# Kernel tuning notes

Measured on AMD Instinct MI355X. Metric: run time of the kernel, lower is better.

## Reference

```python
import jax, jax.numpy as jnp
import numpy as np

B, T, W, HP = 1, 64, 88, 48   # batch, frames, pitches, hidden_per_pitch
NU, NH, K = 24, 4, 25          # n_unit, n_heads, neighborhood window
HD = NU // NH                  # head dim = 6
HL = NU // 2                   # LSTM hidden per direction = 12


def _lstm_bidir(x, w_ih, w_hh, b_ih, b_hh):
    # x: [N, T, In]; w_ih: [2, 4*HL, In]; w_hh: [2, 4*HL, HL]; biases: [2, 4*HL]
    N = x.shape[0]
    def run(Wih, Whh, bih, bhh, reverse):
        def step(carry, xt):
            h, c = carry
            g = xt @ Wih.T + h @ Whh.T + bih + bhh
            i, f, gg, o = jnp.split(g, 4, axis=-1)  # torch gate order i,f,g,o
            c = jax.nn.sigmoid(f) * c + jax.nn.sigmoid(i) * jnp.tanh(gg)
            h = jax.nn.sigmoid(o) * jnp.tanh(c)
            return (h, c), h
        init = (jnp.zeros((N, HL), x.dtype), jnp.zeros((N, HL), x.dtype))
        _, ys = jax.lax.scan(step, init, jnp.swapaxes(x, 0, 1), reverse=reverse)
        return jnp.swapaxes(ys, 0, 1)
    return jnp.concatenate([run(w_ih[0], w_hh[0], b_ih[0], b_hh[0], False),
                            run(w_ih[1], w_hh[1], b_ih[1], b_hh[1], True)], axis=-1)


def _natten2d(x, qkv_w, qkv_b, rpb, proj_w, proj_b):
    # Neighborhood attention over 2D grid [B, Hh, Ww] with KxK window clamped at borders.
    Bn, Hh, Ww, C = x.shape
    qkv = (x @ qkv_w.T + qkv_b).reshape(Bn, Hh, Ww, 3, NH, HD)
    q = qkv[..., 0, :, :] * (HD ** -0.5)
    k = qkv[..., 1, :, :]
    v = qkv[..., 2, :, :]
    half = K // 2
    ar = jnp.arange(K)
    idx_i = jnp.clip(jnp.arange(Hh) - half, 0, Hh - K)[:, None] + ar  # [Hh,K]
    idx_j = jnp.clip(jnp.arange(Ww) - half, 0, Ww - K)[:, None] + ar  # [Ww,K]
    kg = k[:, idx_i][:, :, :, idx_j]  # [B,Hh,K,Ww,K,NH,HD]
    vg = v[:, idx_i][:, :, :, idx_j]
    ri = idx_i - jnp.arange(Hh)[:, None] + (K - 1)  # relative pos bias indices [Hh,K]
    rj = idx_j - jnp.arange(Ww)[:, None] + (K - 1)  # [Ww,K]
    bias = rpb[:, ri][:, :, :, rj]                  # [NH,Hh,K,Ww,K]
    logits = jnp.einsum('bijnd,biajcnd->bnijac', q, kg)
    logits = logits + jnp.transpose(bias, (0, 1, 3, 2, 4))[None]
    attn = jax.nn.softmax(logits.reshape(Bn, NH, Hh, Ww, K * K), axis=-1)
    attn = attn.reshape(Bn, NH, Hh, Ww, K, K)
    out = jnp.einsum('bnijac,biajcnd->bijnd', attn, vg).reshape(Bn, Hh, Ww, C)
    return out @ proj_w.T + proj_b


def _forward(features, condition, mask, emb, w_ih_l0, w_hh_l0, b_ih_l0, b_hh_l0,
             w_ih_l1, w_hh_l1, b_ih_l1, b_hh_l1, qkv_w, qkv_b, rpb, proj_w, proj_b,
             out_w, out_b):
    # concat: [B,T,88,HP] + [B,T,88,4] + [B,T,88,1] -> [B,T,88,HP+5]
    cat = jnp.concatenate([jnp.transpose(features, (0, 1, 3, 2)), emb[condition],
                           mask[..., None]], axis=-1)
    x = jnp.transpose(cat, (0, 2, 1, 3)).reshape(B * W, T, HP + 5)  # pitchwise LSTM
    x = _lstm_bidir(x, w_ih_l0, w_hh_l0, b_ih_l0, b_hh_l0)
    x = _lstm_bidir(x, w_ih_l1, w_hh_l1, b_ih_l1, b_hh_l1)
    x = jnp.transpose(x.reshape(B, W, T, NU), (0, 2, 1, 3))  # [B,T,88,NU]
    for _ in range(2):  # n_layers=2; Sequential(*[m]*2) => SHARED weights
        x = _natten2d(x, qkv_w, qkv_b, rpb, proj_w, proj_b)
    return x @ out_w.T + out_b  # [B,T,88,5]


def setup_inputs():
    ks = jax.random.split(jax.random.key(0), 24)
    def unif(k, shape, fan):
        s = 1.0 / np.sqrt(fan)
        return jax.random.uniform(k, shape, jnp.float32, -s, s)
    return {
        'features': jax.random.normal(ks[0], (B, T, HP, W), jnp.float32),
        'condition': jax.random.randint(ks[1], (B, T, W), 0, 5),
        'mask': jax.random.uniform(ks[2], (B, T, W), jnp.float32),
        'emb': jax.random.normal(ks[3], (5, 4), jnp.float32),
        'w_ih_l0': unif(ks[4], (2, 4 * HL, HP + 5), HL),
        'w_hh_l0': unif(ks[5], (2, 4 * HL, HL), HL),
        'b_ih_l0': unif(ks[6], (2, 4 * HL), HL),
        'b_hh_l0': unif(ks[7], (2, 4 * HL), HL),
        'w_ih_l1': unif(ks[8], (2, 4 * HL, 2 * HL), HL),
        'w_hh_l1': unif(ks[9], (2, 4 * HL, HL), HL),
        'b_ih_l1': unif(ks[10], (2, 4 * HL), HL),
        'b_hh_l1': unif(ks[11], (2, 4 * HL), HL),
        'qkv_w': unif(ks[12], (3 * NU, NU), NU),
        'qkv_b': unif(ks[13], (3 * NU,), NU),
        'rpb': jax.random.normal(ks[14], (NH, 2 * K - 1, 2 * K - 1), jnp.float32) * 0.02,
        'proj_w': unif(ks[15], (NU, NU), NU),
        'proj_b': unif(ks[16], (NU,), NU),
        'out_w': unif(ks[17], (5, NU), NU),
        'out_b': unif(ks[18], (5,), NU),
    }


def reference(features, condition, mask, emb, w_ih_l0, w_hh_l0, b_ih_l0, b_hh_l0,
              w_ih_l1, w_hh_l1, b_ih_l1, b_hh_l1, qkv_w, qkv_b, rpb, proj_w, proj_b,
              out_w, out_b):
    return _forward(features, condition, mask, emb, w_ih_l0, w_hh_l0, b_ih_l0, b_hh_l0,
                    w_ih_l1, w_hh_l1, b_ih_l1, b_hh_l1, qkv_w, qkv_b, rpb,
                    proj_w, proj_b, out_w, out_b)
```

## Files before the change

### kernel.cpp

```cpp
#include <hip/hip_runtime.h>
#include <hip/hip_bf16.h>

#define NPIX (64*88)
#define NSEQ 88
#define TT 64
#define F0 53
#define GATES 48

typedef __hip_bfloat16 bf16;

__device__ __forceinline__ float frcp(float x){ return __builtin_amdgcn_rcpf(x); }

__device__ __forceinline__ void unpack6(uint4 r, float* f){
  f[0] = __uint_as_float(r.x << 16);
  f[1] = __uint_as_float(r.x & 0xffff0000u);
  f[2] = __uint_as_float(r.y << 16);
  f[3] = __uint_as_float(r.y & 0xffff0000u);
  f[4] = __uint_as_float(r.z << 16);
  f[5] = __uint_as_float(r.z & 0xffff0000u);
}

__global__ __launch_bounds__(1024) void k_core(
    const float* __restrict__ feat, const int* __restrict__ cond,
    const float* __restrict__ mask, const float* __restrict__ emb,
    const float* __restrict__ wih0, const float* __restrict__ whh0,
    const float* __restrict__ bih0, const float* __restrict__ bhh0,
    const float* __restrict__ wih1, const float* __restrict__ whh1,
    const float* __restrict__ bih1, const float* __restrict__ bhh1,
    const float* __restrict__ qkv_w, const float* __restrict__ qkv_b,
    float* __restrict__ q, bf16* __restrict__ kh, bf16* __restrict__ vh){
  int n = blockIdx.x; int tid = threadIdx.x;
  int wave = tid >> 6; int lane = tid & 63;
  __shared__ float smem[14816];
  float* gbuf = smem;
  float* sx   = smem + 6144;
  float* sw0  = smem + 6144+3392;
  float* w1   = smem + 6144;
  float* sqkv = smem + 6144+2400;
  float* y0   = smem + 6144+4200;
  float* y1   = smem + 6144+5736;
  float* bsum = smem + 14624;

  for (int idx = tid; idx < 2*GATES*F0; idx += 1024) sw0[idx] = wih0[idx];
  for (int idx = tid; idx < TT*F0; idx += 1024){
    int t = idx / F0, f = idx - t*F0;
    float v;
    if (f < 48)      v = feat[(t*48 + f)*88 + n];
    else if (f < 52) v = emb[cond[t*88+n]*4 + (f-48)];
    else             v = mask[t*88+n];
    sx[idx] = v;
  }
  if (tid < 96)       bsum[tid] = bih0[tid] + bhh0[tid];
  else if (tid < 192) bsum[tid] = bih1[tid-96] + bhh1[tid-96];
  __syncthreads();

  #pragma unroll
  for (int r = 0; r < 6; ++r){
    int row = tid + r*1024;
    int d = row / 3072; int rem = row - d*3072;
    int t = rem / 48; int j = rem - t*48;
    const float* xr = sx + t*F0;
    const float* wr = sw0 + (d*GATES + j)*F0;
    float a0=0.f, a1=0.f, a2=0.f, a3=0.f;
    #pragma unroll
    for (int f=0; f<52; f+=4){
      a0 += xr[f  ]*wr[f  ];
      a1 += xr[f+1]*wr[f+1];
      a2 += xr[f+2]*wr[f+2];
      a3 += xr[f+3]*wr[f+3];
    }
    gbuf[(d*TT + t)*GATES + j] = bsum[d*GATES+j] + xr[52]*wr[52] + ((a0+a1)+(a2+a3));
  }
  __syncthreads();

  if (wave >= 2){
    for (int idx = tid-128; idx < 2*GATES*24; idx += 896){
      int row = idx / 24, f = idx - row*24;
      w1[row*25 + f] = wih1[idx];
    }
    for (int idx = tid-128; idx < 72*24; idx += 896){
      int row = idx / 24, f = idx - row*24;
      sqkv[row*25 + f] = qkv_w[idx];
    }
  } else {
    int d = wave;
    int j = (lane < GATES) ? lane : (lane - GATES);
    int u = j % 12; int grp = j / 12;
    float w[12];
    const float* wb = whh0 + (d*GATES + j)*12;
    #pragma unroll
    for (int m=0;m<12;++m) w[m] = wb[m];
    float negs  = (grp==2) ? -2.f : -1.f;
    float amul  = (grp==2) ?  2.f :  1.f;
    float aadd  = (grp==2) ? -1.f :  0.f;
    const float* gb = gbuf + d*TT*GATES + j;
    float hval = 0.f, cval = 0.f;
    int t0 = d ? (TT-1) : 0;
    float gnext = gb[t0*GATES];
    for (int s=0;s<TT;++s){
      int t = d ? (TT-1-s) : s;
      float gg = gnext;
      int tn = d ? max(TT-2-s,0) : min(s+1,TT-1);
      gnext = gb[tn*GATES];
      float h0=__shfl(hval,0), h1=__shfl(hval,1), h2=__shfl(hval,2);
      float h3=__shfl(hval,3), h4=__shfl(hval,4), h5=__shfl(hval,5);
      float h6=__shfl(hval,6), h7=__shfl(hval,7), h8=__shfl(hval,8);
      float h9=__shfl(hval,9), h10=__shfl(hval,10), h11=__shfl(hval,11);
      float a0 = gg + h0*w[0] + h4*w[4] + h8*w[8];
      float a1 = h1*w[1] + h5*w[5] + h9*w[9];
      float a2 = h2*w[2] + h6*w[6] + h10*w[10];
      float a3 = h3*w[3] + h7*w[7] + h11*w[11];
      float dot = (a0+a1)+(a2+a3);
      float act = amul*frcp(1.f + __expf(negs*dot)) + aadd;
      float ai = __shfl(act, u);
      float af = __shfl(act, u+12);
      float ag = __shfl(act, u+24);
      float ao = __shfl(act, u+36);
      float cn = af*cval + ai*ag;
      float th = 2.f*frcp(1.f + __expf(-2.f*cn)) - 1.f;
      hval = ao*th; cval = cn;
      if (lane < 12) y0[t*24 + d*12 + lane] = hval;
    }
  }
  __syncthreads();

  #pragma unroll
  for (int r = 0; r < 6; ++r){
    int row = tid + r*1024;
    int d = row / 3072; int rem = row - d*3072;
    int t = rem / 48; int j = rem - t*48;
    const float* xr = y0 + t*24;
    const float* wr = w1 + (d*GATES + j)*25;
    float a0=0.f, a1=0.f;
    #pragma unroll
    for (int c=0; c<24; c+=2){ a0 += xr[c]*wr[c]; a1 += xr[c+1]*wr[c+1]; }
    gbuf[(d*TT + t)*GATES + j] = bsum[96 + d*GATES+j] + a0 + a1;
  }
  __syncthreads();

  if (wave < 2){
    int d = wave;
    int j = (lane < GATES) ? lane : (lane - GATES);
    int u = j % 12; int grp = j / 12;
    float w[12];
    const float* wb = whh1 + (d*GATES + j)*12;
    #pragma unroll
    for (int m=0;m<12;++m) w[m] = wb[m];
    float negs  = (grp==2) ? -2.f : -1.f;
    float amul  = (grp==2) ?  2.f :  1.f;
    float aadd  = (grp==2) ? -1.f :  0.f;
    const float* gb = gbuf + d*TT*GATES + j;
    float hval = 0.f, cval = 0.f;
    int t0 = d ? (TT-1) : 0;
    float gnext = gb[t0*GATES];
    for (int s=0;s<TT;++s){
      int t = d ? (TT-1-s) : s;
      float gg = gnext;
      int tn = d ? max(TT-2-s,0) : min(s+1,TT-1);
      gnext = gb[tn*GATES];
      float h0=__shfl(hval,0), h1=__shfl(hval,1), h2=__shfl(hval,2);
      float h3=__shfl(hval,3), h4=__shfl(hval,4), h5=__shfl(hval,5);
      float h6=__shfl(hval,6), h7=__shfl(hval,7), h8=__shfl(hval,8);
      float h9=__shfl(hval,9), h10=__shfl(hval,10), h11=__shfl(hval,11);
      float a0 = gg + h0*w[0] + h4*w[4] + h8*w[8];
      float a1 = h1*w[1] + h5*w[5] + h9*w[9];
      float a2 = h2*w[2] + h6*w[6] + h10*w[10];
      float a3 = h3*w[3] + h7*w[7] + h11*w[11];
      float dot = (a0+a1)+(a2+a3);
      float act = amul*frcp(1.f + __expf(negs*dot)) + aadd;
      float ai = __shfl(act, u);
      float af = __shfl(act, u+12);
      float ag = __shfl(act, u+24);
      float ao = __shfl(act, u+36);
      float cn = af*cval + ai*ag;
      float th = 2.f*frcp(1.f + __expf(-2.f*cn)) - 1.f;
      hval = ao*th; cval = cn;
      if (lane < 12) y1[t*24 + d*12 + lane] = hval;
    }
  }
  __syncthreads();

  for (int idx = tid; idx < TT*72; idx += 1024){
    int gq = idx % 72; int t = idx / 72;
    int p = t*88 + n;
    const float* xr = y1 + t*24;
    const float* wr = sqkv + gq*25;
    float a0=0.f, a1=0.f;
    #pragma unroll
    for (int c=0; c<24; c+=2){ a0 += xr[c]*wr[c]; a1 += xr[c+1]*wr[c+1]; }
    float acc = qkv_b[gq] + a0 + a1;
    int s = gq/24, rem = gq - s*24;
    if (s==0) q[p*24+rem] = acc*0.4082482904638631f;
    else {
      int hh = rem/6, pos = rem - hh*6;
      bf16* dst = (s==1) ? kh : vh;
      dst[((size_t)hh*NPIX + p)*8 + pos] = __float2bfloat16(acc);
    }
  }
}

__global__ __launch_bounds__(512) void k_attn(
    const float* __restrict__ q, const bf16* __restrict__ kh,
    const bf16* __restrict__ vh, const float* __restrict__ rpb,
    float* __restrict__ ao){
  int b = blockIdx.x;
  int h = b / 704; int rem = b - h*704;
  int ti = rem / 44, tj = rem - ti*44;
  int i0 = ti*4, j0 = tj*2;
  int tid = threadIdx.x;
  int w = tid >> 6; int lane = tid & 63;
  int osi = min(max(i0-12,0),39);
  int osj = min(max(j0-12,0),63);

  __shared__ uint4 kt[28*26];
  __shared__ uint4 vt[28*26];
  const uint4* kg = (const uint4*)(kh + (size_t)h*NPIX*8);
  const uint4* vg = (const uint4*)(vh + (size_t)h*NPIX*8);
  for (int idx = tid; idx < 28*26; idx += 512){
    int a = idx / 26, cc = idx - a*26;
    int gi = min(osi + a, 63), gj = min(osj + cc, 87);
    int src = gi*88 + gj;
    kt[idx] = kg[src];
    vt[idx] = vg[src];
  }
  __syncthreads();

  int pi = i0 + (w>>1), pj = j0 + (w&1);
  int p = pi*88 + pj;
  int dsi = min(max(pi-12,0),39) - osi;
  int dsj = min(max(pj-12,0),63) - osj;
  int rbi = osi + dsi - pi + 24;
  int rbj = osj + dsj - pj + 24;

  float qv[6];
  #pragma unroll
  for (int d=0; d<6; ++d) qv[d] = q[p*24 + h*6 + d];

  float lgv[10]; int rof[10];
  float lmax = -1e30f;
  #pragma unroll
  for (int it=0; it<10; ++it){
    int nb = lane + it*64;
    bool valid = nb < 625;
    int nbc = valid ? nb : 624;
    int a = nbc/25, cc = nbc - a*25;
    int r = (a+dsi)*26 + (cc+dsj);
    rof[it] = r;
    float kr[6];
    unpack6(kt[r], kr);
    float lg = qv[0]*kr[0]+qv[1]*kr[1]+qv[2]*kr[2]+qv[3]*kr[3]+qv[4]*kr[4]+qv[5]*kr[5];
    lg += rpb[(h*49 + (a + rbi))*49 + (cc + rbj)];
    lg = valid ? lg : -1e30f;
    lgv[it] = lg;
    lmax = fmaxf(lmax, lg);
  }
  #pragma unroll
  for (int off=32; off; off>>=1) lmax = fmaxf(lmax, __shfl_xor(lmax, off));
  float lsum = 0.f;
  #pragma unroll
  for (int it=0; it<10; ++it){
    float pe = __expf(lgv[it]-lmax);
    lgv[it] = pe; lsum += pe;
  }
  #pragma unroll
  for (int off=32; off; off>>=1) lsum += __shfl_xor(lsum, off);
  float acc[6] = {0,0,0,0,0,0};
  #pragma unroll
  for (int it=0; it<10; ++it){
    float vr[6];
    unpack6(vt[rof[it]], vr);
    float pe = lgv[it];
    #pragma unroll
    for (int d=0; d<6; ++d) acc[d] += pe*vr[d];
  }
  #pragma unroll
  for (int d=0; d<6; ++d){
    #pragma unroll
    for (int off=32; off; off>>=1) acc[d] += __shfl_xor(acc[d], off);
  }
  if (lane == 0){
    float inv = frcp(lsum);
    #pragma unroll
    for (int d=0; d<6; ++d) ao[p*24 + h*6 + d] = acc[d]*inv;
  }
}

__global__ __launch_bounds__(64) void k_proj_qkv(const float* __restrict__ ain,
    const float* __restrict__ pw, const float* __restrict__ pb,
    const float* __restrict__ qkv_w, const float* __restrict__ qkv_b,
    float* __restrict__ q2, bf16* __restrict__ kh2, bf16* __restrict__ vh2){
  int p = blockIdx.x; int tid = threadIdx.x;
  __shared__ float arow[24];
  __shared__ float xrow[24];
  if (tid < 24) arow[tid] = ain[p*24+tid];
  __syncthreads();
  if (tid < 24){
    float a2 = pb[tid];
    const float* wr = pw + tid*24;
    #pragma unroll
    for (int c=0;c<24;++c) a2 += arow[c]*wr[c];
    xrow[tid] = a2;
  }
  __syncthreads();
  for (int g = tid; g < 72; g += 64){
    float a2 = qkv_b[g];
    const float* wr = qkv_w + g*24;
    #pragma unroll
    for (int c=0;c<24;++c) a2 += xrow[c]*wr[c];
    int s = g/24, rem = g - s*24;
    if (s==0) q2[p*24+rem] = a2*0.4082482904638631f;
    else {
      int hh = rem/6, pos = rem - hh*6;
      bf16* dst = (s==1) ? kh2 : vh2;
      dst[((size_t)hh*NPIX + p)*8 + pos] = __float2bfloat16(a2);
    }
  }
}

__global__ __launch_bounds__(64) void k_proj_out(const float* __restrict__ ain,
    const float* __restrict__ pw, const float* __restrict__ pb,
    const float* __restrict__ ow, const float* __restrict__ ob,
    float* __restrict__ out){
  int p = blockIdx.x; int tid = threadIdx.x;
  __shared__ float arow[24];
  __shared__ float xrow[24];
  if (tid < 24) arow[tid] = ain[p*24+tid];
  __syncthreads();
  if (tid < 24){
    float a2 = pb[tid];
    const float* wr = pw + tid*24;
    #pragma unroll
    for (int c=0;c<24;++c) a2 += arow[c]*wr[c];
    xrow[tid] = a2;
  }
  __syncthreads();
  if (tid < 5){
    float a2 = ob[tid];
    const float* wr = ow + tid*24;
    #pragma unroll
    for (int c=0;c<24;++c) a2 += xrow[c]*wr[c];
    out[p*5+tid] = a2;
  }
}

extern "C" void kernel_launch(void* const* d_in, const int* in_sizes, int n_in,
                              void* d_out, int out_size, void* d_ws, size_t ws_size,
                              hipStream_t stream) {
  const float* feat    = (const float*)d_in[0];
  const int*   cond    = (const int*)  d_in[1];
  const float* mask    = (const float*)d_in[2];
  const float* emb     = (const float*)d_in[3];
  const float* w_ih_l0 = (const float*)d_in[4];
  const float* w_hh_l0 = (const float*)d_in[5];
  const float* b_ih_l0 = (const float*)d_in[6];
  const float* b_hh_l0 = (const float*)d_in[7];
  const float* w_ih_l1 = (const float*)d_in[8];
  const float* w_hh_l1 = (const float*)d_in[9];
  const float* b_ih_l1 = (const float*)d_in[10];
  const float* b_hh_l1 = (const float*)d_in[11];
  const float* qkv_w   = (const float*)d_in[12];
  const float* qkv_b   = (const float*)d_in[13];
  const float* rpb     = (const float*)d_in[14];
  const float* proj_w  = (const float*)d_in[15];
  const float* proj_b  = (const float*)d_in[16];
  const float* out_w   = (const float*)d_in[17];
  const float* out_b   = (const float*)d_in[18];
  float* out = (float*)d_out;

  float* ws  = (float*)d_ws;
  float* Q1  = ws;
  float* Q2  = Q1 + 135168;
  float* AO  = Q2 + 135168;
  bf16*  KH1 = (bf16*)(AO + 135168);
  bf16*  VH1 = KH1 + 180224;
  bf16*  KH2 = VH1 + 180224;
  bf16*  VH2 = KH2 + 180224;

  k_core<<<NSEQ, 1024, 0, stream>>>(
      feat, cond, mask, emb,
      w_ih_l0, w_hh_l0, b_ih_l0, b_hh_l0,
      w_ih_l1, w_hh_l1, b_ih_l1, b_hh_l1,
      qkv_w, qkv_b, Q1, KH1, VH1);

  k_attn<<<4*16*44, 512, 0, stream>>>(Q1, KH1, VH1, rpb, AO);

  k_proj_qkv<<<NPIX, 64, 0, stream>>>(AO, proj_w, proj_b, qkv_w, qkv_b,
                                      Q2, KH2, VH2);

  k_attn<<<4*16*44, 512, 0, stream>>>(Q2, KH2, VH2, rpb, AO);

  k_proj_out<<<NPIX, 64, 0, stream>>>(AO, proj_w, proj_b, out_w, out_b, out);
}
```

Baseline: 210.3 us.

## Fuse neighborhood attention with projection and next QKV/output linear layers

The attention kernel now handles all 4 heads for a 4x2 pixel tile in one 1024-thread block, then applies the output projection and either the next layer's QKV projection or the final 5-way output head in-block. This removes the separate per-pixel projection kernels, the AO round trip through global memory, and two launches. K is staged in LDS for all heads while V is now read straight from global memory, trading LDS footprint for global-load latency. k_core's block-to-sequence mapping is also permuted.

```diff
diff --git a/kernel.cpp b/kernel.cpp
--- a/kernel.cpp
+++ b/kernel.cpp
@@ -29,7 +29,8 @@
     const float* __restrict__ bih1, const float* __restrict__ bhh1,
     const float* __restrict__ qkv_w, const float* __restrict__ qkv_b,
     float* __restrict__ q, bf16* __restrict__ kh, bf16* __restrict__ vh){
-  int n = blockIdx.x; int tid = threadIdx.x;
+  int n = (blockIdx.x & 7)*11 + (blockIdx.x >> 3);
+  int tid = threadIdx.x;
   int wave = tid >> 6; int lane = tid & 63;
   __shared__ float smem[14816];
   float* gbuf = smem;
@@ -199,45 +200,50 @@
   }
 }
 
-__global__ __launch_bounds__(512) void k_attn(
+__global__ __launch_bounds__(1024) void k_attn_fused(
     const float* __restrict__ q, const bf16* __restrict__ kh,
     const bf16* __restrict__ vh, const float* __restrict__ rpb,
-    float* __restrict__ ao){
+    const float* __restrict__ pw, const float* __restrict__ pb,
+    const float* __restrict__ qkv_w, const float* __restrict__ qkv_b,
+    float* __restrict__ q2, bf16* __restrict__ kh2, bf16* __restrict__ vh2,
+    const float* __restrict__ ow, const float* __restrict__ ob,
+    float* __restrict__ out, int last){
   int b = blockIdx.x;
-  int h = b / 704; int rem = b - h*704;
-  int ti = rem / 44, tj = rem - ti*44;
+  int ti = b / 44, tj = b - ti*44;
   int i0 = ti*4, j0 = tj*2;
   int tid = threadIdx.x;
   int w = tid >> 6; int lane = tid & 63;
   int osi = min(max(i0-12,0),39);
   int osj = min(max(j0-12,0),63);
 
-  __shared__ uint4 kt[28*26];
-  __shared__ uint4 vt[28*26];
-  const uint4* kg = (const uint4*)(kh + (size_t)h*NPIX*8);
-  const uint4* vg = (const uint4*)(vh + (size_t)h*NPIX*8);
-  for (int idx = tid; idx < 28*26; idx += 512){
-    int a = idx / 26, cc = idx - a*26;
+  __shared__ uint4 kt[4*728];
+  __shared__ float aorow[8][24];
+  __shared__ float xrow[8][24];
+
+  for (int idx = tid; idx < 4*728; idx += 1024){
+    int hh = idx / 728; int r = idx - hh*728;
+    int a = r / 26, cc = r - a*26;
     int gi = min(osi + a, 63), gj = min(osj + cc, 87);
-    int src = gi*88 + gj;
-    kt[idx] = kg[src];
-    vt[idx] = vg[src];
-  }
-  __syncthreads();
-
-  int pi = i0 + (w>>1), pj = j0 + (w&1);
+    kt[idx] = ((const uint4*)(kh + (size_t)hh*NPIX*8))[gi*88 + gj];
+  }
+  __syncthreads();
+
+  int pl = w >> 1;
+  int hp = (w & 1) * 2;
+  int pi = i0 + (pl >> 1), pj = j0 + (pl & 1);
   int p = pi*88 + pj;
-  int dsi = min(max(pi-12,0),39) - osi;
-  int dsj = min(max(pj-12,0),63) - osj;
-  int rbi = osi + dsi - pi + 24;
-  int rbj = osj + dsj - pj + 24;
-
-  float qv[6];
-  #pragma unroll
-  for (int d=0; d<6; ++d) qv[d] = q[p*24 + h*6 + d];
-
-  float lgv[10]; int rof[10];
-  float lmax = -1e30f;
+  int si = min(max(pi-12,0),39), sj = min(max(pj-12,0),63);
+  int dsi = si - osi, dsj = sj - osj;
+  int rbi = si - pi + 24, rbj = sj - pj + 24;
+
+  float qv[12];
+  #pragma unroll
+  for (int hh=0; hh<2; ++hh)
+    #pragma unroll
+    for (int d=0; d<6; ++d) qv[hh*6+d] = q[p*24 + (hp+hh)*6 + d];
+
+  float lgv[2][10];
+  float mx[2] = {-1e30f,-1e30f};
   #pragma unroll
   for (int it=0; it<10; ++it){
     int nb = lane + it*64;
@@ -245,101 +251,104 @@
     int nbc = valid ? nb : 624;
     int a = nbc/25, cc = nbc - a*25;
     int r = (a+dsi)*26 + (cc+dsj);
-    rof[it] = r;
-    float kr[6];
-    unpack6(kt[r], kr);
-    float lg = qv[0]*kr[0]+qv[1]*kr[1]+qv[2]*kr[2]+qv[3]*kr[3]+qv[4]*kr[4]+qv[5]*kr[5];
-    lg += rpb[(h*49 + (a + rbi))*49 + (cc + rbj)];
-    lg = valid ? lg : -1e30f;
-    lgv[it] = lg;
-    lmax = fmaxf(lmax, lg);
-  }
-  #pragma unroll
-  for (int off=32; off; off>>=1) lmax = fmaxf(lmax, __shfl_xor(lmax, off));
-  float lsum = 0.f;
+    #pragma unroll
+    for (int hh=0; hh<2; ++hh){
+      float kr[6];
+      unpack6(kt[(hp+hh)*728 + r], kr);
+      float lg = qv[hh*6+0]*kr[0]+qv[hh*6+1]*kr[1]+qv[hh*6+2]*kr[2]
+               + qv[hh*6+3]*kr[3]+qv[hh*6+4]*kr[4]+qv[hh*6+5]*kr[5];
+      lg += rpb[((hp+hh)*49 + (a + rbi))*49 + (cc + rbj)];
+      lg = valid ? lg : -1e30f;
+      lgv[hh][it] = lg;
+      mx[hh] = fmaxf(mx[hh], lg);
+    }
+  }
+  #pragma unroll
+  for (int hh=0; hh<2; ++hh)
+    #pragma unroll
+    for (int off=32; off; off>>=1) mx[hh] = fmaxf(mx[hh], __shfl_xor(mx[hh], off));
+  float sm[2] = {0.f, 0.f};
+  #pragma unroll
+  for (int it=0; it<10; ++it)
+    #pragma unroll
+    for (int hh=0; hh<2; ++hh){
+      float pe = __expf(lgv[hh][it]-mx[hh]);
+      lgv[hh][it] = pe; sm[hh] += pe;
+    }
+  #pragma unroll
+  for (int hh=0; hh<2; ++hh)
+    #pragma unroll
+    for (int off=32; off; off>>=1) sm[hh] += __shfl_xor(sm[hh], off);
+
+  float acc[12];
+  #pragma unroll
+  for (int u=0; u<12; ++u) acc[u] = 0.f;
   #pragma unroll
   for (int it=0; it<10; ++it){
-    float pe = __expf(lgv[it]-lmax);
-    lgv[it] = pe; lsum += pe;
-  }
-  #pragma unroll
-  for (int off=32; off; off>>=1) lsum += __shfl_xor(lsum, off);
-  float acc[6] = {0,0,0,0,0,0};
-  #pragma unroll
-  for (int it=0; it<10; ++it){
-    float vr[6];
-    unpack6(vt[rof[it]], vr);
-    float pe = lgv[it];
-    #pragma unroll
-    for (int d=0; d<6; ++d) acc[d] += pe*vr[d];
-  }
-  #pragma unroll
-  for (int d=0; d<6; ++d){
-    #pragma unroll
-    for (int off=32; off; off>>=1) acc[d] += __shfl_xor(acc[d], off);
-  }
+    int nb = lane + it*64;
+    int nbc = (nb < 625) ? nb : 624;
+    int a = nbc/25, cc = nbc - a*25;
+    int grow = (si + a)*88 + (sj + cc);
+    #pragma unroll
+    for (int hh=0; hh<2; ++hh){
+      float vr[6];
+      unpack6(((const uint4*)(vh + (size_t)(hp+hh)*NPIX*8))[grow], vr);
+      float pe = lgv[hh][it];
+      #pragma unroll
+      for (int d=0; d<6; ++d) acc[hh*6+d] += pe*vr[d];
+    }
+  }
+  #pragma unroll
+  for (int u=0; u<12; ++u)
+    #pragma unroll
+    for (int off=32; off; off>>=1) acc[u] += __shfl_xor(acc[u], off);
+
   if (lane == 0){
-    float inv = frcp(lsum);
-    #pragma unroll
-    for (int d=0; d<6; ++d) ao[p*24 + h*6 + d] = acc[d]*inv;
-  }
-}
-
-__global__ __launch_bounds__(64) void k_proj_qkv(const float* __restrict__ ain,
-    const float* __restrict__ pw, const float* __restrict__ pb,
-    const float* __restrict__ qkv_w, const float* __restrict__ qkv_b,
-    float* __restrict__ q2, bf16* __restrict__ kh2, bf16* __restrict__ vh2){
-  int p = blockIdx.x; int tid = threadIdx.x;
-  __shared__ float arow[24];
-  __shared__ float xrow[24];
-  if (tid < 24) arow[tid] = ain[p*24+tid];
-  __syncthreads();
-  if (tid < 24){
-    float a2 = pb[tid];
-    const float* wr = pw + tid*24;
-    #pragma unroll
-    for (int c=0;c<24;++c) a2 += arow[c]*wr[c];
-    xrow[tid] = a2;
-  }
-  __syncthreads();
-  for (int g = tid; g < 72; g += 64){
-    float a2 = qkv_b[g];
-    const float* wr = qkv_w + g*24;
-    #pragma unroll
-    for (int c=0;c<24;++c) a2 += xrow[c]*wr[c];
-    int s = g/24, rem = g - s*24;
-    if (s==0) q2[p*24+rem] = a2*0.4082482904638631f;
-    else {
-      int hh = rem/6, pos = rem - hh*6;
-      bf16* dst = (s==1) ? kh2 : vh2;
-      dst[((size_t)hh*NPIX + p)*8 + pos] = __float2bfloat16(a2);
-    }
-  }
-}
-
-__global__ __launch_bounds__(64) void k_proj_out(const float* __restrict__ ain,
-    const float* __restrict__ pw, const float* __restrict__ pb,
-    const float* __restrict__ ow, const float* __restrict__ ob,
-    float* __restrict__ out){
-  int p = blockIdx.x; int tid = threadIdx.x;
-  __shared__ float arow[24];
-  __shared__ float xrow[24];
-  if (tid < 24) arow[tid] = ain[p*24+tid];
-  __syncthreads();
-  if (tid < 24){
-    float a2 = pb[tid];
-    const float* wr = pw + tid*24;
-    #pragma unroll
-    for (int c=0;c<24;++c) a2 += arow[c]*wr[c];
-    xrow[tid] = a2;
-  }
-  __syncthreads();
-  if (tid < 5){
-    float a2 = ob[tid];
-    const float* wr = ow + tid*24;
-    #pragma unroll
-    for (int c=0;c<24;++c) a2 += xrow[c]*wr[c];
-    out[p*5+tid] = a2;
+    float i0v = frcp(sm[0]), i1v = frcp(sm[1]);
+    #pragma unroll
+    for (int d=0; d<6; ++d){
+      aorow[pl][hp*6 + d]     = acc[d]*i0v;
+      aorow[pl][(hp+1)*6 + d] = acc[6+d]*i1v;
+    }
+  }
+  __syncthreads();
+
+  if (tid < 192){
+    int pp = tid / 24, o = tid - pp*24;
+    float a2 = pb[o];
+    const float* wr = pw + o*24;
+    #pragma unroll
+    for (int c=0;c<24;++c) a2 += aorow[pp][c]*wr[c];
+    xrow[pp][o] = a2;
+  }
+  __syncthreads();
+
+  if (!last){
+    if (tid < 576){
+      int pp = tid / 72, g = tid - pp*72;
+      int pg = (i0 + (pp>>1))*88 + (j0 + (pp&1));
+      float a2 = qkv_b[g];
+      const float* wr = qkv_w + g*24;
+      #pragma unroll
+      for (int c=0;c<24;++c) a2 += xrow[pp][c]*wr[c];
+      int s = g/24, rem = g - s*24;
+      if (s==0) q2[pg*24+rem] = a2*0.4082482904638631f;
+      else {
+        int hh = rem/6, pos = rem - hh*6;
+        bf16* dst = (s==1) ? kh2 : vh2;
+        dst[((size_t)hh*NPIX + pg)*8 + pos] = __float2bfloat16(a2);
+      }
+    }
+  } else {
+    if (tid < 40){
+      int pp = tid / 5, o = tid - pp*5;
+      int pg = (i0 + (pp>>1))*88 + (j0 + (pp&1));
+      float a2 = ob[o];
+      const float* wr = ow + o*24;
+      #pragma unroll
+      for (int c=0;c<24;++c) a2 += xrow[pp][c]*wr[c];
+      out[pg*5+o] = a2;
+    }
   }
 }
 
@@ -370,8 +379,7 @@
   float* ws  = (float*)d_ws;
   float* Q1  = ws;
   float* Q2  = Q1 + 135168;
-  float* AO  = Q2 + 135168;
-  bf16*  KH1 = (bf16*)(AO + 135168);
+  bf16*  KH1 = (bf16*)(Q2 + 135168);
   bf16*  VH1 = KH1 + 180224;
   bf16*  KH2 = VH1 + 180224;
   bf16*  VH2 = KH2 + 180224;
@@ -382,12 +390,11 @@
       w_ih_l1, w_hh_l1, b_ih_l1, b_hh_l1,
       qkv_w, qkv_b, Q1, KH1, VH1);
 
-  k_attn<<<4*16*44, 512, 0, stream>>>(Q1, KH1, VH1, rpb, AO);
-
-  k_proj_qkv<<<NPIX, 64, 0, stream>>>(AO, proj_w, proj_b, qkv_w, qkv_b,
-                                      Q2, KH2, VH2);
-
-  k_attn<<<4*16*44, 512, 0, stream>>>(Q2, KH2, VH2, rpb, AO);
-
-  k_proj_out<<<NPIX, 64, 0, stream>>>(AO, proj_w, proj_b, out_w, out_b, out);
+  k_attn_fused<<<16*44, 1024, 0, stream>>>(
+      Q1, KH1, VH1, rpb, proj_w, proj_b, qkv_w, qkv_b,
+      Q2, KH2, VH2, out_w, out_b, out, 0);
+
+  k_attn_fused<<<16*44, 1024, 0, stream>>>(
+      Q2, KH2, VH2, rpb, proj_w, proj_b, qkv_w, qkv_b,
+      Q1, KH1, VH1, out_w, out_b, out, 1);
 }
```

After: 309.6 us. +47.2%, slower.
